# Performance work log

Hardware: AMD Instinct MI355X
Metric: run time of the kernel (lower is better)

The kernel has to match this reference:

```python
import jax, jax.numpy as jnp
import numpy as np
import itertools, math

METRIC = [1.0, 1.0, 1.0]  # Cl(3,0)
EPS = 1e-6
SQRT2 = math.sqrt(2.0)


def _build_algebra(metric):
    d = len(metric)
    # basis blades ordered by grade, then lexicographic combination (repo convention)
    blades = []
    for g in range(d + 1):
        for c in itertools.combinations(range(d), g):
            blades.append(sum(1 << i for i in c))
    idx = {m: i for i, m in enumerate(blades)}
    n = len(blades)
    C = np.zeros((n, n, n), dtype=np.float32)  # cayley[i, j, k]: e_i * e_k -> sign * e_j
    for ia, am in enumerate(blades):
        for ik, bm in enumerate(blades):
            a = am >> 1
            swaps = 0
            while a:
                swaps += bin(a & bm).count('1')
                a >>= 1
            sign = -1.0 if (swaps & 1) else 1.0
            for i in range(d):
                if am & bm & (1 << i):
                    sign *= metric[i]
            C[ia, idx[am ^ bm], ik] = sign
    grades = np.array([bin(m).count('1') for m in blades])
    subspaces = np.array([int((grades == g).sum()) for g in range(d + 1)])
    paths = np.zeros((d + 1, d + 1, d + 1), dtype=bool)
    for i in range(d + 1):
        for j in range(d + 1):
            for k in range(d + 1):
                paths[i, j, k] = np.any(C[np.ix_(grades == i, grades == j, grades == k)] != 0)
    return C, subspaces, paths, grades

CAYLEY_NP, SUBSPACES, PATHS, GRADE_OF_COMP = _build_algebra(METRIC)
REP_IDX = np.repeat(np.arange(len(SUBSPACES)), SUBSPACES)  # component -> grade, len 8
PI, PJ, PK = np.nonzero(PATHS)                              # 20 active grade triples
ONEHOT_GRADE = np.eye(len(SUBSPACES), dtype=np.float32)[GRADE_OF_COMP]  # [8,4]

B, N_IN, N_OUT = 1024, 256, 256
DIM_MV = CAYLEY_NP.shape[0]  # 8
N_PATHS = int(PATHS.sum())   # 20


def mv_linear(x, w, bias=None):
    # MVLinear: per-grade weight repeated over components; einsum 'bm...i,nmi->bn...i'
    wr = w[:, :, REP_IDX]                       # [out, in, 8]
    out = jnp.einsum('bmi,nmi->bni', x, wr)
    if bias is not None:
        out = out.at[:, :, 0].add(bias[:, :, 0])  # bias embedded in scalar (grade-0) slot
    return out


def normalize_mv(x, a):
    # per-grade norms (Euclidean metric => L2 norm of each grade block)
    oh = jnp.asarray(ONEHOT_GRADE)
    norms = jnp.sqrt(jnp.einsum('bni,ig->bng', x * x, oh))  # [b, n, 4]
    interp = jax.nn.sigmoid(a)[None] * (norms - 1.0) + 1.0  # learned interp toward unit norm
    return x / (interp[:, :, REP_IDX] + EPS)


def gp_kernel(gp_weight):
    # scatter 20 path weights into (m, n, 4, 4, 4), repeat per subspace, mask by cayley
    m, n, _ = gp_weight.shape
    g = len(SUBSPACES)
    w4 = jnp.zeros((m, n, g, g, g), gp_weight.dtype).at[:, :, PI, PJ, PK].set(gp_weight)
    wrep = w4[:, :, REP_IDX][:, :, :, REP_IDX][:, :, :, :, REP_IDX]  # [m, n, 8, 8, 8]
    return jnp.asarray(CAYLEY_NP)[None, None] * wrep


def setup_inputs() -> dict:
    key = jax.random.key(0)
    ks = jax.random.split(key, 5)
    std_gp = 1.0 / math.sqrt(N_IN * (len(METRIC) + 1))
    std_lin = 1.0 / math.sqrt(N_IN)
    return {
        'x': jax.random.normal(ks[0], (B, N_IN, DIM_MV), jnp.float32),
        'w_right': jax.random.normal(ks[1], (N_IN, N_IN, len(SUBSPACES)), jnp.float32) * std_lin,
        'w_left': jax.random.normal(ks[2], (N_OUT, N_IN, len(SUBSPACES)), jnp.float32) * std_lin,
        'b_left': jax.random.normal(ks[3], (1, N_OUT, 1), jnp.float32) * 0.02,
        'norm_a': jnp.zeros((N_IN, len(SUBSPACES)), jnp.float32),  # normalization_init = 0
        'gp_weight': jax.random.normal(ks[4], (N_OUT, N_IN, N_PATHS), jnp.float32) * std_gp,
    }


def reference(x, w_right, w_left, b_left, norm_a, gp_weight):
    x_right = normalize_mv(mv_linear(x, w_right), norm_a)
    kernel = gp_kernel(gp_weight)                 # [m, n, 8, 8, 8]
    outer = jnp.einsum('bni,bnk->bnik', x, x_right)  # [b, n, 8, 8]
    prod = jnp.einsum('bnik,mnijk->bmj', outer, kernel)
    left = mv_linear(x, w_left, b_left)
    return (left + prod) / SQRT2
```

## Files before the change

kernel.cpp:

```cpp
#include <hip/hip_runtime.h>
#include <math.h>

typedef unsigned short ushortT;
typedef __bf16 bf16x8 __attribute__((ext_vector_type(8)));
typedef float  f32x4  __attribute__((ext_vector_type(4)));

__constant__ int GRADEc[8] = {0,1,1,1,2,2,2,3};

__constant__ int CMAPc[8][7] = {
  {0, 8, 9,10,11, 0, 0},
  {1,12,13,14,15,16,17},
  {2,18,19,20,21,22,23},
  {3,24,25,26,27,28,29},
  {4,30,31,32,33,34,35},
  {5,36,37,38,39,40,41},
  {6,42,43,44,45,46,47},
  {7,48,49,50,51, 0, 0}};
__constant__ int WMAPc[8][7] = {
  {0, 4, 8,14,20, 0, 0},
  {1, 5, 9,10,15,16,21},
  {1, 5, 9,10,15,16,21},
  {1, 5, 9,10,15,16,21},
  {2, 6,11,12,17,18,22},
  {2, 6,11,12,17,18,22},
  {2, 6,11,12,17,18,22},
  {3, 7,13,19,23, 0, 0}};
__constant__ int SSTART2c[8][2] = {{0,3},{0,4},{0,4},{0,4},{0,4},{0,4},{0,4},{0,3}};
__constant__ int SCOUNT2c[8][2] = {{3,2},{4,3},{4,3},{4,3},{4,3},{4,3},{4,3},{3,2}};

__device__ __forceinline__ ushortT f2bf(float f) {
  unsigned int u = __float_as_uint(f);
  unsigned int r = (u + 0x7fffu + ((u >> 16) & 1u)) >> 16;
  return (ushortT)r;
}

#define GLOAD_LDS16(gsrc, ldst) \
  __builtin_amdgcn_global_load_lds((const __attribute__((address_space(1))) unsigned int*)(gsrc), \
                                   (__attribute__((address_space(3))) unsigned int*)(ldst), 16, 0, 0)

#define WAITVM(N) asm volatile("s_waitcnt vmcnt(" #N ")" ::: "memory")
#define SCHEDB()  __builtin_amdgcn_sched_barrier(0)
#define RAWBAR()  do { SCHEDB(); __builtin_amdgcn_s_barrier(); asm volatile("" ::: "memory"); SCHEDB(); } while (0)

__global__ void k_prep(const float* __restrict__ x, const float* __restrict__ w_right,
                       const float* __restrict__ w_left, const float* __restrict__ gp,
                       ushortT* __restrict__ XH, ushortT* __restrict__ XL,
                       ushortT* __restrict__ WH, ushortT* __restrict__ WL,
                       ushortT* __restrict__ WT2b) {
  const int bid = blockIdx.x;
  const int tid = threadIdx.x;
  if (bid < 256) {
    const int m = bid, n = tid;
    float4 wl = *(const float4*)(w_left + m * 1024 + n * 4);
    float g[20];
    const float4* gp4 = (const float4*)(gp + m * 5120 + n * 20);
    #pragma unroll
    for (int q = 0; q < 5; ++q) {
      float4 v = gp4[q];
      g[q * 4 + 0] = v.x; g[q * 4 + 1] = v.y; g[q * 4 + 2] = v.z; g[q * 4 + 3] = v.w;
    }
    const int base = m * 256 + n;
    WT2b[0 * 65536 + base] = f2bf(wl.x);
    WT2b[1 * 65536 + base] = f2bf(wl.y);
    WT2b[2 * 65536 + base] = f2bf(wl.z);
    WT2b[3 * 65536 + base] = f2bf(wl.w);
    #pragma unroll
    for (int p = 0; p < 20; ++p)
      WT2b[(4 + p) * 65536 + base] = f2bf(g[p]);
  } else if (bid < 1280) {
    int b = bid - 256;
    const float4* xp = (const float4*)(x + b * 2048 + tid * 8);
    float4 a = xp[0], c = xp[1];
    float v[8] = {a.x, a.y, a.z, a.w, c.x, c.y, c.z, c.w};
    #pragma unroll
    for (int i = 0; i < 8; ++i) {
      ushortT h = f2bf(v[i]);
      float hf = __uint_as_float(((unsigned int)h) << 16);
      XH[i * 262144 + b * 256 + tid] = h;
      XL[i * 262144 + b * 256 + tid] = f2bf(v[i] - hf);
    }
  } else {
    int n = bid - 1280;
    float4 w = *(const float4*)(w_right + n * 1024 + tid * 4);
    float v[4] = {w.x, w.y, w.z, w.w};
    #pragma unroll
    for (int g2 = 0; g2 < 4; ++g2) {
      ushortT h = f2bf(v[g2]);
      float hf = __uint_as_float(((unsigned int)h) << 16);
      WH[g2 * 65536 + n * 256 + tid] = h;
      WL[g2 * 65536 + n * 256 + tid] = f2bf(v[g2] - hf);
    }
  }
}

__global__ __launch_bounds__(512) void k_right_feat(const ushortT* __restrict__ XH,
                                                    const ushortT* __restrict__ XL,
                                                    const ushortT* __restrict__ WH,
                                                    const ushortT* __restrict__ WL,
                                                    const float* __restrict__ x,
                                                    const float* __restrict__ norm_a,
                                                    ushortT* __restrict__ FT2b) {
  const int lin = blockIdx.x;
  const int rr  = lin & 7;
  const int q   = lin >> 3;
  const int xb  = q & 7;
  const int yb  = (q >> 3) * 8 + rr;
  const int n0 = xb * 32;
  const int b0 = yb * 32;
  __shared__ __align__(16) ushortT lds[49152];
  const int t    = threadIdx.x;
  const int wave = t >> 6;
  const int lane = t & 63;
  const int i    = wave;
  const int g    = GRADEc[i];
  const int lrow = lane & 15, lkg = lane >> 4;
  const int srow = lane >> 2;
  const int sseg = lane & 3;

  const ushortT* Asrc_h = XH + i * 262144 + b0 * 256;
  const ushortT* Asrc_l = XL + i * 262144 + b0 * 256;
  const int bg = wave >> 1;
  const ushortT* Bsrc = ((wave & 1) ? WL : WH) + bg * 65536 + n0 * 256;

  f32x4 acc[2][2];
  #pragma unroll
  for (int r = 0; r < 2; ++r)
    #pragma unroll
    for (int c = 0; c < 2; ++c)
      acc[r][c] = (f32x4){0.f, 0.f, 0.f, 0.f};

  auto STAGE = [&](int k0, int buf) {
    ushortT* base = lds + buf * 24576;
    #pragma unroll
    for (int q2 = 0; q2 < 2; ++q2) {
      int row = q2 * 16 + srow;
      int slog = sseg ^ ((row >> 1) & 3);
      GLOAD_LDS16(Asrc_h + row * 256 + k0 + slog * 8, base + i * 1024 + q2 * 512);
      GLOAD_LDS16(Asrc_l + row * 256 + k0 + slog * 8, base + 8192 + i * 1024 + q2 * 512);
      GLOAD_LDS16(Bsrc   + row * 256 + k0 + slog * 8,
                  base + 16384 + (wave & 1) * 4096 + bg * 1024 + q2 * 512);
    }
  };

  auto COMPUTE = [&](int buf) {
    const ushortT* base = lds + buf * 24576;
    bf16x8 afh[2], afl[2], bfh[2], bfl[2];
    #pragma unroll
    for (int r = 0; r < 2; ++r) {
      int row = r * 16 + lrow;
      int po = row * 32 + (lkg ^ ((row >> 1) & 3)) * 8;
      afh[r] = *(const bf16x8*)(base + i * 1024 + po);
      afl[r] = *(const bf16x8*)(base + 8192 + i * 1024 + po);
    }
    #pragma unroll
    for (int c = 0; c < 2; ++c) {
      int row = c * 16 + lrow;
      int po = row * 32 + (lkg ^ ((row >> 1) & 3)) * 8;
      bfh[c] = *(const bf16x8*)(base + 16384 + g * 1024 + po);
      bfl[c] = *(const bf16x8*)(base + 20480 + g * 1024 + po);
    }
    #pragma unroll
    for (int r = 0; r < 2; ++r)
      #pragma unroll
      for (int c = 0; c < 2; ++c) {
        acc[r][c] = __builtin_amdgcn_mfma_f32_16x16x32_bf16(afh[r], bfh[c], acc[r][c], 0, 0, 0);
        acc[r][c] = __builtin_amdgcn_mfma_f32_16x16x32_bf16(afl[r], bfh[c], acc[r][c], 0, 0, 0);
        acc[r][c] = __builtin_amdgcn_mfma_f32_16x16x32_bf16(afh[r], bfl[c], acc[r][c], 0, 0, 0);
      }
  };

  STAGE(0, 0);
  int cur = 0;
  for (int tc = 0; tc < 8; ++tc) {
    if (tc < 7) { STAGE((tc + 1) * 32, cur ^ 1); SCHEDB(); WAITVM(6); }
    else        { WAITVM(0); }
    RAWBAR();
    COMPUTE(cur);
    if (tc < 7) RAWBAR();
    cur ^= 1;
  }

  float* yl = (float*)lds;
  #pragma unroll
  for (int r = 0; r < 2; ++r)
    #pragma unroll
    for (int c = 0; c < 2; ++c)
      #pragma unroll
      for (int e = 0; e < 4; ++e) {
        int row = r * 16 + lkg * 4 + e;
        int col = c * 16 + lrow;
        yl[i * 1056 + row * 33 + col] = acc[r][c][e];
      }
  __syncthreads();

  #pragma unroll
  for (int e2 = 0; e2 < 2; ++e2) {
    int el  = t + e2 * 512;
    int row = el >> 5, col = el & 31;
    int b = b0 + row, n = n0 + col;
    float y[8];
    #pragma unroll
    for (int q2 = 0; q2 < 8; ++q2) y[q2] = yl[q2 * 1056 + row * 33 + col];
    const float4* xp = (const float4*)(x + b * 2048 + n * 8);
    float4 x01 = xp[0], x23 = xp[1];
    float xv[8] = {x01.x, x01.y, x01.z, x01.w, x23.x, x23.y, x23.z, x23.w};
    float4 na = *(const float4*)(norm_a + n * 4);
    float nav[4] = {na.x, na.y, na.z, na.w};
    float nr[4];
    nr[0] = fabsf(y[0]);
    nr[1] = sqrtf(y[1]*y[1] + y[2]*y[2] + y[3]*y[3]);
    nr[2] = sqrtf(y[4]*y[4] + y[5]*y[5] + y[6]*y[6]);
    nr[3] = fabsf(y[7]);
    float inv[4];
    #pragma unroll
    for (int gg = 0; gg < 4; ++gg) {
      float s = 1.0f / (1.0f + expf(-nav[gg]));
      inv[gg] = 1.0f / (s * (nr[gg] - 1.0f) + 1.0f + 1e-6f);
    }
    float r[8];
    r[0] = y[0]*inv[0];
    r[1] = y[1]*inv[1]; r[2] = y[2]*inv[1]; r[3] = y[3]*inv[1];
    r[4] = y[4]*inv[2]; r[5] = y[5]*inv[2]; r[6] = y[6]*inv[2];
    r[7] = y[7]*inv[3];

    float F[52];
    F[8]  = xv[0]*r[0];
    F[9]  = xv[1]*r[1] + xv[2]*r[2] + xv[3]*r[3];
    F[10] = -(xv[4]*r[4] + xv[5]*r[5] + xv[6]*r[6]);
    F[11] = -xv[7]*r[7];
    F[12] = xv[0]*r[1];
    F[13] = xv[1]*r[0];
    F[14] = -(xv[2]*r[4] + xv[3]*r[5]);
    F[15] = xv[4]*r[2] + xv[5]*r[3];
    F[16] = -xv[6]*r[7];
    F[17] = -xv[7]*r[6];
    F[18] = xv[0]*r[2];
    F[19] = xv[2]*r[0];
    F[20] = xv[1]*r[4] - xv[3]*r[6];
    F[21] = -xv[4]*r[1] + xv[6]*r[3];
    F[22] = xv[5]*r[7];
    F[23] = xv[7]*r[5];
    F[24] = xv[0]*r[3];
    F[25] = xv[3]*r[0];
    F[26] = xv[1]*r[5] + xv[2]*r[6];
    F[27] = -(xv[5]*r[1] + xv[6]*r[2]);
    F[28] = -xv[4]*r[7];
    F[29] = -xv[7]*r[4];
    F[30] = xv[0]*r[4];
    F[31] = xv[1]*r[2] - xv[2]*r[1];
    F[32] = xv[3]*r[7];
    F[33] = xv[4]*r[0];
    F[34] = -xv[5]*r[6] + xv[6]*r[5];
    F[35] = xv[7]*r[3];
    F[36] = xv[0]*r[5];
    F[37] = xv[1]*r[3] - xv[3]*r[1];
    F[38] = -xv[2]*r[7];
    F[39] = xv[5]*r[0];
    F[40] = xv[4]*r[6] - xv[6]*r[4];
    F[41] = -xv[7]*r[2];
    F[42] = xv[0]*r[6];
    F[43] = xv[2]*r[3] - xv[3]*r[2];
    F[44] = xv[1]*r[7];
    F[45] = xv[6]*r[0];
    F[46] = -xv[4]*r[5] + xv[5]*r[4];
    F[47] = xv[7]*r[1];
    F[48] = xv[0]*r[7];
    F[49] = xv[1]*r[6] - xv[2]*r[5] + xv[3]*r[4];
    F[50] = xv[4]*r[3] - xv[5]*r[2] + xv[6]*r[1];
    F[51] = xv[7]*r[0];

    #pragma unroll
    for (int c = 8; c < 52; ++c)
      FT2b[c * 262144 + b * 256 + n] = f2bf(F[c]);
  }
}

__global__ __launch_bounds__(512) void k_gemm_mfma(const ushortT* __restrict__ XH,
                                                   const ushortT* __restrict__ FT2b,
                                                   const ushortT* __restrict__ WT2b,
                                                   float* __restrict__ outP) {
  const int lin = blockIdx.x;
  const int rr  = lin & 7;
  const int q   = lin >> 3;
  const int ix  = q & 15;
  const int z   = rr + 8 * (q >> 4);
  const int j   = z >> 1;
  const int ks  = z & 1;
  const int m0  = (ix & 1) * 128;
  const int b0  = (ix >> 1) * 128;
  __shared__ __align__(16) ushortT lds[32768];
  const int t    = threadIdx.x;
  const int wave = t >> 6;
  const int kkg  = wave >> 2;
  const int w4   = wave & 3;
  const int lane = t & 63;
  const int wb   = (w4 & 1) * 64;
  const int wm   = (w4 >> 1) * 64;
  const int lrow = lane & 15;
  const int lkg  = lane >> 4;
  const int srow = lane >> 3;
  const int sseg = lane & 7;

  f32x4 acc[4][4];
  #pragma unroll
  for (int r = 0; r < 4; ++r)
    #pragma unroll
    for (int c = 0; c < 4; ++c)
      acc[r][c] = (f32x4){0.f, 0.f, 0.f, 0.f};

  const int sstart = SSTART2c[j][ks];
  const int nt     = SCOUNT2c[j][ks] * 4;

  auto STAGE = [&](int tch, int buf) {
    int slot = sstart + (tch >> 2);
    int k0   = (tch & 3) << 6;
    const ushortT* Ap = ((slot == 0) ? (XH + j * 262144)
                                     : (FT2b + CMAPc[j][slot] * 262144)) + b0 * 256;
    const ushortT* Bp = WT2b + WMAPc[j][slot] * 65536 + m0 * 256;
    #pragma unroll
    for (int q2 = 0; q2 < 2; ++q2) {
      int idx = wave * 2 + q2;
      int row = idx * 8 + srow;
      int slog = sseg ^ (row & 7);
      GLOAD_LDS16(Ap + row * 256 + k0 + slog * 8, lds + buf * 8192 + idx * 512);
      GLOAD_LDS16(Bp + row * 256 + k0 + slog * 8, lds + 16384 + buf * 8192 + idx * 512);
    }
  };

  STAGE(0, 0);
  int cur = 0;
  for (int tc = 0; tc < nt; ++tc) {
    if (tc + 1 < nt) { STAGE(tc + 1, cur ^ 1); SCHEDB(); WAITVM(4); }
    else             { WAITVM(0); }
    RAWBAR();
    const ushortT* sA = lds + cur * 8192;
    const ushortT* sB = lds + 16384 + cur * 8192;
    bf16x8 af[4], bf[4];
    #pragma unroll
    for (int r = 0; r < 4; ++r) {
      int row = wb + r * 16 + lrow;
      af[r] = *(const bf16x8*)(sA + row * 64 + (((kkg * 4 + lkg) ^ (row & 7)) * 8));
    }
    #pragma unroll
    for (int c = 0; c < 4; ++c) {
      int row = wm + c * 16 + lrow;
      bf[c] = *(const bf16x8*)(sB + row * 64 + (((kkg * 4 + lkg) ^ (row & 7)) * 8));
    }
    #pragma unroll
    for (int r = 0; r < 4; ++r)
      #pragma unroll
      for (int c = 0; c < 4; ++c)
        acc[r][c] = __builtin_amdgcn_mfma_f32_16x16x32_bf16(af[r], bf[c], acc[r][c], 0, 0, 0);
    if (tc + 1 < nt) RAWBAR();
    cur ^= 1;
  }

  __syncthreads();
  float* fl = (float*)lds;
  if (kkg == 1) {
    #pragma unroll
    for (int r = 0; r < 4; ++r)
      #pragma unroll
      for (int c = 0; c < 4; ++c)
        #pragma unroll
        for (int e = 0; e < 4; ++e) {
          int row = r * 16 + lkg * 4 + e;
          int col = c * 16 + lrow;
          fl[w4 * 4096 + row * 64 + col] = acc[r][c][e];
        }
  }
  __syncthreads();
  if (kkg == 0) {
    float* oj = outP + (ks * 8 + j) * 262144;
    #pragma unroll
    for (int r = 0; r < 4; ++r) {
      #pragma unroll
      for (int c = 0; c < 4; ++c) {
        #pragma unroll
        for (int e = 0; e < 4; ++e) {
          int row = r * 16 + lkg * 4 + e;
          int col = c * 16 + lrow;
          float v = acc[r][c][e] + fl[w4 * 4096 + row * 64 + col];
          oj[(b0 + wb + row) * 256 + m0 + wm + col] = v;
        }
      }
    }
  }
}

__global__ void k_merge(const float* __restrict__ outP, const float* __restrict__ bleft,
                        float* __restrict__ out) {
  const int t4 = (blockIdx.x * 256 + threadIdx.x) * 4;
  const int m  = t4 & 255;
  const float sc = 0.7071067811865475f;
  float o[4][8];
  #pragma unroll
  for (int jj = 0; jj < 8; ++jj) {
    float4 s = make_float4(0.f, 0.f, 0.f, 0.f);
    #pragma unroll
    for (int p = 0; p < 2; ++p) {
      float4 v = *(const float4*)(outP + (p * 8 + jj) * 262144 + t4);
      s.x += v.x; s.y += v.y; s.z += v.z; s.w += v.w;
    }
    o[0][jj] = s.x; o[1][jj] = s.y; o[2][jj] = s.z; o[3][jj] = s.w;
  }
  #pragma unroll
  for (int q = 0; q < 4; ++q) {
    float ov[8];
    #pragma unroll
    for (int jj = 0; jj < 8; ++jj) ov[jj] = o[q][jj];
    ov[0] += bleft[m + q];
    float4 v0 = make_float4(ov[0]*sc, ov[1]*sc, ov[2]*sc, ov[3]*sc);
    float4 v1 = make_float4(ov[4]*sc, ov[5]*sc, ov[6]*sc, ov[7]*sc);
    *(float4*)(out + (t4 + q) * 8)     = v0;
    *(float4*)(out + (t4 + q) * 8 + 4) = v1;
  }
}

extern "C" void kernel_launch(void* const* d_in, const int* in_sizes, int n_in,
                              void* d_out, int out_size, void* d_ws, size_t ws_size,
                              hipStream_t stream) {
  const float* x       = (const float*)d_in[0];
  const float* w_right = (const float*)d_in[1];
  const float* w_left  = (const float*)d_in[2];
  const float* b_left  = (const float*)d_in[3];
  const float* norm_a  = (const float*)d_in[4];
  const float* gp      = (const float*)d_in[5];
  float* out = (float*)d_out;
  float* W   = (float*)d_ws;

  float*   outP = W;
  ushortT* XH   = (ushortT*)(W + 4194304);
  ushortT* XL   = (ushortT*)(W + 5242880);
  ushortT* WH   = (ushortT*)(W + 6291456);
  ushortT* WL   = (ushortT*)(W + 6422528);
  ushortT* FT2b = (ushortT*)(W + 6553600);
  ushortT* WT2b = (ushortT*)(W + 13369344);

  k_prep<<<1536, 256, 0, stream>>>(x, w_right, w_left, gp, XH, XL, WH, WL, WT2b);
  k_right_feat<<<256, 512, 0, stream>>>(XH, XL, WH, WL, x, norm_a, FT2b);
  k_gemm_mfma<<<256, 512, 0, stream>>>(XH, FT2b, WT2b, outP);
  k_merge<<<256, 256, 0, stream>>>(outP, b_left, out);
}
```

Baseline: 109.9 us.

## Fuse four kernels into one cooperative kernel with grid syncs

Merges the prep, right-feature GEMM, main GEMM and merge kernels into a single cooperative launch of 256 blocks of 512 threads, separated by grid-wide barriers. This removes three kernel launch gaps and the tail/ramp between stages. In exchange, the prep and merge stages run with fewer, larger blocks doing strided loops, all stages share one LDS allocation sized for the largest, and grid.sync adds barrier cost.

```diff
diff --git a/kernel.cpp b/kernel.cpp
--- a/kernel.cpp
+++ b/kernel.cpp
@@ -1,5 +1,8 @@
 #include <hip/hip_runtime.h>
+#include <hip/hip_cooperative_groups.h>
 #include <math.h>
+
+namespace cg = cooperative_groups;
 
 typedef unsigned short ushortT;
 typedef __bf16 bf16x8 __attribute__((ext_vector_type(8)));
@@ -42,378 +45,386 @@
 #define SCHEDB()  __builtin_amdgcn_sched_barrier(0)
 #define RAWBAR()  do { SCHEDB(); __builtin_amdgcn_s_barrier(); asm volatile("" ::: "memory"); SCHEDB(); } while (0)
 
-__global__ void k_prep(const float* __restrict__ x, const float* __restrict__ w_right,
-                       const float* __restrict__ w_left, const float* __restrict__ gp,
-                       ushortT* __restrict__ XH, ushortT* __restrict__ XL,
-                       ushortT* __restrict__ WH, ushortT* __restrict__ WL,
-                       ushortT* __restrict__ WT2b) {
+__global__ __launch_bounds__(512, 2) void k_fused(
+    const float* __restrict__ x, const float* __restrict__ w_right,
+    const float* __restrict__ w_left, const float* __restrict__ bleft,
+    const float* __restrict__ norm_a, const float* __restrict__ gp,
+    float* __restrict__ out,
+    ushortT* __restrict__ XH, ushortT* __restrict__ XL,
+    ushortT* __restrict__ WH, ushortT* __restrict__ WL,
+    ushortT* __restrict__ FT2b, ushortT* __restrict__ WT2b,
+    float* __restrict__ outP) {
+  cg::grid_group grid = cg::this_grid();
+  __shared__ __align__(16) ushortT lds[49152];
   const int bid = blockIdx.x;
   const int tid = threadIdx.x;
-  if (bid < 256) {
-    const int m = bid, n = tid;
-    float4 wl = *(const float4*)(w_left + m * 1024 + n * 4);
-    float g[20];
-    const float4* gp4 = (const float4*)(gp + m * 5120 + n * 20);
+
+  {
     #pragma unroll
-    for (int q = 0; q < 5; ++q) {
-      float4 v = gp4[q];
-      g[q * 4 + 0] = v.x; g[q * 4 + 1] = v.y; g[q * 4 + 2] = v.z; g[q * 4 + 3] = v.w;
-    }
-    const int base = m * 256 + n;
-    WT2b[0 * 65536 + base] = f2bf(wl.x);
-    WT2b[1 * 65536 + base] = f2bf(wl.y);
-    WT2b[2 * 65536 + base] = f2bf(wl.z);
-    WT2b[3 * 65536 + base] = f2bf(wl.w);
-    #pragma unroll
-    for (int p = 0; p < 20; ++p)
-      WT2b[(4 + p) * 65536 + base] = f2bf(g[p]);
-  } else if (bid < 1280) {
-    int b = bid - 256;
-    const float4* xp = (const float4*)(x + b * 2048 + tid * 8);
-    float4 a = xp[0], c = xp[1];
-    float v[8] = {a.x, a.y, a.z, a.w, c.x, c.y, c.z, c.w};
-    #pragma unroll
-    for (int i = 0; i < 8; ++i) {
-      ushortT h = f2bf(v[i]);
-      float hf = __uint_as_float(((unsigned int)h) << 16);
-      XH[i * 262144 + b * 256 + tid] = h;
-      XL[i * 262144 + b * 256 + tid] = f2bf(v[i] - hf);
-    }
-  } else {
-    int n = bid - 1280;
-    float4 w = *(const float4*)(w_right + n * 1024 + tid * 4);
-    float v[4] = {w.x, w.y, w.z, w.w};
-    #pragma unroll
-    for (int g2 = 0; g2 < 4; ++g2) {
-      ushortT h = f2bf(v[g2]);
-      float hf = __uint_as_float(((unsigned int)h) << 16);
-      WH[g2 * 65536 + n * 256 + tid] = h;
-      WL[g2 * 65536 + n * 256 + tid] = f2bf(v[g2] - hf);
+    for (int k = 0; k < 3; ++k) {
+      int u  = k * 131072 + bid * 512 + tid;
+      int vb = u >> 8, vt = u & 255;
+      if (vb < 256) {
+        const int m = vb, n = vt;
+        float4 wl = *(const float4*)(w_left + m * 1024 + n * 4);
+        float g[20];
+        const float4* gp4 = (const float4*)(gp + m * 5120 + n * 20);
+        #pragma unroll
+        for (int q = 0; q < 5; ++q) {
+          float4 v = gp4[q];
+          g[q * 4 + 0] = v.x; g[q * 4 + 1] = v.y; g[q * 4 + 2] = v.z; g[q * 4 + 3] = v.w;
+        }
+        const int base = m * 256 + n;
+        WT2b[0 * 65536 + base] = f2bf(wl.x);
+        WT2b[1 * 65536 + base] = f2bf(wl.y);
+        WT2b[2 * 65536 + base] = f2bf(wl.z);
+        WT2b[3 * 65536 + base] = f2bf(wl.w);
+        #pragma unroll
+        for (int p = 0; p < 20; ++p)
+          WT2b[(4 + p) * 65536 + base] = f2bf(g[p]);
+      } else if (vb < 1280) {
+        int b = vb - 256;
+        const float4* xp = (const float4*)(x + b * 2048 + vt * 8);
+        float4 a = xp[0], c = xp[1];
+        float v[8] = {a.x, a.y, a.z, a.w, c.x, c.y, c.z, c.w};
+        #pragma unroll
+        for (int i = 0; i < 8; ++i) {
+          ushortT h = f2bf(v[i]);
+          float hf = __uint_as_float(((unsigned int)h) << 16);
+          XH[i * 262144 + b * 256 + vt] = h;
+          XL[i * 262144 + b * 256 + vt] = f2bf(v[i] - hf);
+        }
+      } else {
+        int n = vb - 1280;
+        float4 w = *(const float4*)(w_right + n * 1024 + vt * 4);
+        float v[4] = {w.x, w.y, w.z, w.w};
+        #pragma unroll
+        for (int g2 = 0; g2 < 4; ++g2) {
+          ushortT h = f2bf(v[g2]);
+          float hf = __uint_as_float(((unsigned int)h) << 16);
+          WH[g2 * 65536 + n * 256 + vt] = h;
+          WL[g2 * 65536 + n * 256 + vt] = f2bf(v[g2] - hf);
+        }
+      }
     }
   }
-}
-
-__global__ __launch_bounds__(512) void k_right_feat(const ushortT* __restrict__ XH,
-                                                    const ushortT* __restrict__ XL,
-                                                    const ushortT* __restrict__ WH,
-                                                    const ushortT* __restrict__ WL,
-                                                    const float* __restrict__ x,
-                                                    const float* __restrict__ norm_a,
-                                                    ushortT* __restrict__ FT2b) {
-  const int lin = blockIdx.x;
-  const int rr  = lin & 7;
-  const int q   = lin >> 3;
-  const int xb  = q & 7;
-  const int yb  = (q >> 3) * 8 + rr;
-  const int n0 = xb * 32;
-  const int b0 = yb * 32;
-  __shared__ __align__(16) ushortT lds[49152];
-  const int t    = threadIdx.x;
-  const int wave = t >> 6;
-  const int lane = t & 63;
-  const int i    = wave;
-  const int g    = GRADEc[i];
-  const int lrow = lane & 15, lkg = lane >> 4;
-  const int srow = lane >> 2;
-  const int sseg = lane & 3;
-
-  const ushortT* Asrc_h = XH + i * 262144 + b0 * 256;
-  const ushortT* Asrc_l = XL + i * 262144 + b0 * 256;
-  const int bg = wave >> 1;
-  const ushortT* Bsrc = ((wave & 1) ? WL : WH) + bg * 65536 + n0 * 256;
-
-  f32x4 acc[2][2];
-  #pragma unroll
-  for (int r = 0; r < 2; ++r)
-    #pragma unroll
-    for (int c = 0; c < 2; ++c)
-      acc[r][c] = (f32x4){0.f, 0.f, 0.f, 0.f};
-
-  auto STAGE = [&](int k0, int buf) {
-    ushortT* base = lds + buf * 24576;
-    #pragma unroll
-    for (int q2 = 0; q2 < 2; ++q2) {
-      int row = q2 * 16 + srow;
-      int slog = sseg ^ ((row >> 1) & 3);
-      GLOAD_LDS16(Asrc_h + row * 256 + k0 + slog * 8, base + i * 1024 + q2 * 512);
-      GLOAD_LDS16(Asrc_l + row * 256 + k0 + slog * 8, base + 8192 + i * 1024 + q2 * 512);
-      GLOAD_LDS16(Bsrc   + row * 256 + k0 + slog * 8,
-                  base + 16384 + (wave & 1) * 4096 + bg * 1024 + q2 * 512);
-    }
-  };
-
-  auto COMPUTE = [&](int buf) {
-    const ushortT* base = lds + buf * 24576;
-    bf16x8 afh[2], afl[2], bfh[2], bfl[2];
-    #pragma unroll
-    for (int r = 0; r < 2; ++r) {
-      int row = r * 16 + lrow;
-      int po = row * 32 + (lkg ^ ((row >> 1) & 3)) * 8;
-      afh[r] = *(const bf16x8*)(base + i * 1024 + po);
-      afl[r] = *(const bf16x8*)(base + 8192 + i * 1024 + po);
-    }
-    #pragma unroll
-    for (int c = 0; c < 2; ++c) {
-      int row = c * 16 + lrow;
-      int po = row * 32 + (lkg ^ ((row >> 1) & 3)) * 8;
-      bfh[c] = *(const bf16x8*)(base + 16384 + g * 1024 + po);
-      bfl[c] = *(const bf16x8*)(base + 20480 + g * 1024 + po);
-    }
+  grid.sync();
+
+  {
+    const int lin = bid;
+    const int rr  = lin & 7;
+    const int q   = lin >> 3;
+    const int xb  = q & 7;
+    const int yb  = (q >> 3) * 8 + rr;
+    const int n0 = xb * 32;
+    const int b0 = yb * 32;
+    const int t    = tid;
+    const int wave = t >> 6;
+    const int lane = t & 63;
+    const int i    = wave;
+    const int g    = GRADEc[i];
+    const int lrow = lane & 15, lkg = lane >> 4;
+    const int srow = lane >> 2;
+    const int sseg = lane & 3;
+
+    const ushortT* Asrc_h = XH + i * 262144 + b0 * 256;
+    const ushortT* Asrc_l = XL + i * 262144 + b0 * 256;
+    const int bg = wave >> 1;
+    const ushortT* Bsrc = ((wave & 1) ? WL : WH) + bg * 65536 + n0 * 256;
+
+    f32x4 acc[2][2];
     #pragma unroll
     for (int r = 0; r < 2; ++r)
       #pragma unroll
+      for (int c = 0; c < 2; ++c)
+        acc[r][c] = (f32x4){0.f, 0.f, 0.f, 0.f};
+
+    auto STAGE = [&](int k0, int buf) {
+      ushortT* base = lds + buf * 24576;
+      #pragma unroll
+      for (int q2 = 0; q2 < 2; ++q2) {
+        int row = q2 * 16 + srow;
+        int slog = sseg ^ ((row >> 1) & 3);
+        GLOAD_LDS16(Asrc_h + row * 256 + k0 + slog * 8, base + i * 1024 + q2 * 512);
+        GLOAD_LDS16(Asrc_l + row * 256 + k0 + slog * 8, base + 8192 + i * 1024 + q2 * 512);
+        GLOAD_LDS16(Bsrc   + row * 256 + k0 + slog * 8,
+                    base + 16384 + (wave & 1) * 4096 + bg * 1024 + q2 * 512);
+      }
+    };
+
+    auto COMPUTE = [&](int buf) {
+      const ushortT* base = lds + buf * 24576;
+      bf16x8 afh[2], afl[2], bfh[2], bfl[2];
+      #pragma unroll
+      for (int r = 0; r < 2; ++r) {
+        int row = r * 16 + lrow;
+        int po = row * 32 + (lkg ^ ((row >> 1) & 3)) * 8;
+        afh[r] = *(const bf16x8*)(base + i * 1024 + po);
+        afl[r] = *(const bf16x8*)(base + 8192 + i * 1024 + po);
+      }
+      #pragma unroll
       for (int c = 0; c < 2; ++c) {
-        acc[r][c] = __builtin_amdgcn_mfma_f32_16x16x32_bf16(afh[r], bfh[c], acc[r][c], 0, 0, 0);
-        acc[r][c] = __builtin_amdgcn_mfma_f32_16x16x32_bf16(afl[r], bfh[c], acc[r][c], 0, 0, 0);
-        acc[r][c] = __builtin_amdgcn_mfma_f32_16x16x32_bf16(afh[r], bfl[c], acc[r][c], 0, 0, 0);
-      }
-  };
-
-  STAGE(0, 0);
-  int cur = 0;
-  for (int tc = 0; tc < 8; ++tc) {
-    if (tc < 7) { STAGE((tc + 1) * 32, cur ^ 1); SCHEDB(); WAITVM(6); }
-    else        { WAITVM(0); }
-    RAWBAR();
-    COMPUTE(cur);
-    if (tc < 7) RAWBAR();
-    cur ^= 1;
-  }
-
-  float* yl = (float*)lds;
-  #pragma unroll
-  for (int r = 0; r < 2; ++r)
+        int row = c * 16 + lrow;
+        int po = row * 32 + (lkg ^ ((row >> 1) & 3)) * 8;
+        bfh[c] = *(const bf16x8*)(base + 16384 + g * 1024 + po);
+        bfl[c] = *(const bf16x8*)(base + 20480 + g * 1024 + po);
+      }
+      #pragma unroll
+      for (int r = 0; r < 2; ++r)
+        #pragma unroll
+        for (int c = 0; c < 2; ++c) {
+          acc[r][c] = __builtin_amdgcn_mfma_f32_16x16x32_bf16(afh[r], bfh[c], acc[r][c], 0, 0, 0);
+          acc[r][c] = __builtin_amdgcn_mfma_f32_16x16x32_bf16(afl[r], bfh[c], acc[r][c], 0, 0, 0);
+          acc[r][c] = __builtin_amdgcn_mfma_f32_16x16x32_bf16(afh[r], bfl[c], acc[r][c], 0, 0, 0);
+        }
+    };
+
+    STAGE(0, 0);
+    int cur = 0;
+    for (int tc = 0; tc < 8; ++tc) {
+      if (tc < 7) { STAGE((tc + 1) * 32, cur ^ 1); SCHEDB(); WAITVM(6); }
+      else        { WAITVM(0); }
+      RAWBAR();
+      COMPUTE(cur);
+      if (tc < 7) RAWBAR();
+      cur ^= 1;
+    }
+
+    float* yl = (float*)lds;
     #pragma unroll
-    for (int c = 0; c < 2; ++c)
-      #pragma unroll
-      for (int e = 0; e < 4; ++e) {
-        int row = r * 16 + lkg * 4 + e;
-        int col = c * 16 + lrow;
-        yl[i * 1056 + row * 33 + col] = acc[r][c][e];
-      }
-  __syncthreads();
-
-  #pragma unroll
-  for (int e2 = 0; e2 < 2; ++e2) {
-    int el  = t + e2 * 512;
-    int row = el >> 5, col = el & 31;
-    int b = b0 + row, n = n0 + col;
-    float y[8];
-    #pragma unroll
-    for (int q2 = 0; q2 < 8; ++q2) y[q2] = yl[q2 * 1056 + row * 33 + col];
-    const float4* xp = (const float4*)(x + b * 2048 + n * 8);
-    float4 x01 = xp[0], x23 = xp[1];
-    float xv[8] = {x01.x, x01.y, x01.z, x01.w, x23.x, x23.y, x23.z, x23.w};
-    float4 na = *(const float4*)(norm_a + n * 4);
-    float nav[4] = {na.x, na.y, na.z, na.w};
-    float nr[4];
-    nr[0] = fabsf(y[0]);
-    nr[1] = sqrtf(y[1]*y[1] + y[2]*y[2] + y[3]*y[3]);
-    nr[2] = sqrtf(y[4]*y[4] + y[5]*y[5] + y[6]*y[6]);
-    nr[3] = fabsf(y[7]);
-    float inv[4];
-    #pragma unroll
-    for (int gg = 0; gg < 4; ++gg) {
-      float s = 1.0f / (1.0f + expf(-nav[gg]));
-      inv[gg] = 1.0f / (s * (nr[gg] - 1.0f) + 1.0f + 1e-6f);
-    }
-    float r[8];
-    r[0] = y[0]*inv[0];
-    r[1] = y[1]*inv[1]; r[2] = y[2]*inv[1]; r[3] = y[3]*inv[1];
-    r[4] = y[4]*inv[2]; r[5] = y[5]*inv[2]; r[6] = y[6]*inv[2];
-    r[7] = y[7]*inv[3];
-
-    float F[52];
-    F[8]  = xv[0]*r[0];
-    F[9]  = xv[1]*r[1] + xv[2]*r[2] + xv[3]*r[3];
-    F[10] = -(xv[4]*r[4] + xv[5]*r[5] + xv[6]*r[6]);
-    F[11] = -xv[7]*r[7];
-    F[12] = xv[0]*r[1];
-    F[13] = xv[1]*r[0];
-    F[14] = -(xv[2]*r[4] + xv[3]*r[5]);
-    F[15] = xv[4]*r[2] + xv[5]*r[3];
-    F[16] = -xv[6]*r[7];
-    F[17] = -xv[7]*r[6];
-    F[18] = xv[0]*r[2];
-    F[19] = xv[2]*r[0];
-    F[20] = xv[1]*r[4] - xv[3]*r[6];
-    F[21] = -xv[4]*r[1] + xv[6]*r[3];
-    F[22] = xv[5]*r[7];
-    F[23] = xv[7]*r[5];
-    F[24] = xv[0]*r[3];
-    F[25] = xv[3]*r[0];
-    F[26] = xv[1]*r[5] + xv[2]*r[6];
-    F[27] = -(xv[5]*r[1] + xv[6]*r[2]);
-    F[28] = -xv[4]*r[7];
-    F[29] = -xv[7]*r[4];
-    F[30] = xv[0]*r[4];
-    F[31] = xv[1]*r[2] - xv[2]*r[1];
-    F[32] = xv[3]*r[7];
-    F[33] = xv[4]*r[0];
-    F[34] = -xv[5]*r[6] + xv[6]*r[5];
-    F[35] = xv[7]*r[3];
-    F[36] = xv[0]*r[5];
-    F[37] = xv[1]*r[3] - xv[3]*r[1];
-    F[38] = -xv[2]*r[7];
-    F[39] = xv[5]*r[0];
-    F[40] = xv[4]*r[6] - xv[6]*r[4];
-    F[41] = -xv[7]*r[2];
-    F[42] = xv[0]*r[6];
-    F[43] = xv[2]*r[3] - xv[3]*r[2];
-    F[44] = xv[1]*r[7];
-    F[45] = xv[6]*r[0];
-    F[46] = -xv[4]*r[5] + xv[5]*r[4];
-    F[47] = xv[7]*r[1];
-    F[48] = xv[0]*r[7];
-    F[49] = xv[1]*r[6] - xv[2]*r[5] + xv[3]*r[4];
-    F[50] = xv[4]*r[3] - xv[5]*r[2] + xv[6]*r[1];
-    F[51] = xv[7]*r[0];
-
-    #pragma unroll
-    for (int c = 8; c < 52; ++c)
-      FT2b[c * 262144 + b * 256 + n] = f2bf(F[c]);
-  }
-}
-
-__global__ __launch_bounds__(512) void k_gemm_mfma(const ushortT* __restrict__ XH,
-                                                   const ushortT* __restrict__ FT2b,
-                                                   const ushortT* __restrict__ WT2b,
-                                                   float* __restrict__ outP) {
-  const int lin = blockIdx.x;
-  const int rr  = lin & 7;
-  const int q   = lin >> 3;
-  const int ix  = q & 15;
-  const int z   = rr + 8 * (q >> 4);
-  const int j   = z >> 1;
-  const int ks  = z & 1;
-  const int m0  = (ix & 1) * 128;
-  const int b0  = (ix >> 1) * 128;
-  __shared__ __align__(16) ushortT lds[32768];
-  const int t    = threadIdx.x;
-  const int wave = t >> 6;
-  const int kkg  = wave >> 2;
-  const int w4   = wave & 3;
-  const int lane = t & 63;
-  const int wb   = (w4 & 1) * 64;
-  const int wm   = (w4 >> 1) * 64;
-  const int lrow = lane & 15;
-  const int lkg  = lane >> 4;
-  const int srow = lane >> 3;
-  const int sseg = lane & 7;
-
-  f32x4 acc[4][4];
-  #pragma unroll
-  for (int r = 0; r < 4; ++r)
-    #pragma unroll
-    for (int c = 0; c < 4; ++c)
-      acc[r][c] = (f32x4){0.f, 0.f, 0.f, 0.f};
-
-  const int sstart = SSTART2c[j][ks];
-  const int nt     = SCOUNT2c[j][ks] * 4;
-
-  auto STAGE = [&](int tch, int buf) {
-    int slot = sstart + (tch >> 2);
-    int k0   = (tch & 3) << 6;
-    const ushortT* Ap = ((slot == 0) ? (XH + j * 262144)
-                                     : (FT2b + CMAPc[j][slot] * 262144)) + b0 * 256;
-    const ushortT* Bp = WT2b + WMAPc[j][slot] * 65536 + m0 * 256;
-    #pragma unroll
-    for (int q2 = 0; q2 < 2; ++q2) {
-      int idx = wave * 2 + q2;
-      int row = idx * 8 + srow;
-      int slog = sseg ^ (row & 7);
-      GLOAD_LDS16(Ap + row * 256 + k0 + slog * 8, lds + buf * 8192 + idx * 512);
-      GLOAD_LDS16(Bp + row * 256 + k0 + slog * 8, lds + 16384 + buf * 8192 + idx * 512);
-    }
-  };
-
-  STAGE(0, 0);
-  int cur = 0;
-  for (int tc = 0; tc < nt; ++tc) {
-    if (tc + 1 < nt) { STAGE(tc + 1, cur ^ 1); SCHEDB(); WAITVM(4); }
-    else             { WAITVM(0); }
-    RAWBAR();
-    const ushortT* sA = lds + cur * 8192;
-    const ushortT* sB = lds + 16384 + cur * 8192;
-    bf16x8 af[4], bf[4];
-    #pragma unroll
-    for (int r = 0; r < 4; ++r) {
-      int row = wb + r * 16 + lrow;
-      af[r] = *(const bf16x8*)(sA + row * 64 + (((kkg * 4 + lkg) ^ (row & 7)) * 8));
-    }
-    #pragma unroll
-    for (int c = 0; c < 4; ++c) {
-      int row = wm + c * 16 + lrow;
-      bf[c] = *(const bf16x8*)(sB + row * 64 + (((kkg * 4 + lkg) ^ (row & 7)) * 8));
-    }
-    #pragma unroll
-    for (int r = 0; r < 4; ++r)
-      #pragma unroll
-      for (int c = 0; c < 4; ++c)
-        acc[r][c] = __builtin_amdgcn_mfma_f32_16x16x32_bf16(af[r], bf[c], acc[r][c], 0, 0, 0);
-    if (tc + 1 < nt) RAWBAR();
-    cur ^= 1;
-  }
-
-  __syncthreads();
-  float* fl = (float*)lds;
-  if (kkg == 1) {
-    #pragma unroll
-    for (int r = 0; r < 4; ++r)
-      #pragma unroll
-      for (int c = 0; c < 4; ++c)
+    for (int r = 0; r < 2; ++r)
+      #pragma unroll
+      for (int c = 0; c < 2; ++c)
         #pragma unroll
         for (int e = 0; e < 4; ++e) {
           int row = r * 16 + lkg * 4 + e;
           int col = c * 16 + lrow;
-          fl[w4 * 4096 + row * 64 + col] = acc[r][c][e];
-        }
+          yl[i * 1056 + row * 33 + col] = acc[r][c][e];
+        }
+    __syncthreads();
+
+    #pragma unroll
+    for (int e2 = 0; e2 < 2; ++e2) {
+      int el  = t + e2 * 512;
+      int row = el >> 5, col = el & 31;
+      int b = b0 + row, n = n0 + col;
+      float y[8];
+      #pragma unroll
+      for (int q2 = 0; q2 < 8; ++q2) y[q2] = yl[q2 * 1056 + row * 33 + col];
+      const float4* xp = (const float4*)(x + b * 2048 + n * 8);
+      float4 x01 = xp[0], x23 = xp[1];
+      float xv[8] = {x01.x, x01.y, x01.z, x01.w, x23.x, x23.y, x23.z, x23.w};
+      float4 na = *(const float4*)(norm_a + n * 4);
+      float nav[4] = {na.x, na.y, na.z, na.w};
+      float nr[4];
+      nr[0] = fabsf(y[0]);
+      nr[1] = sqrtf(y[1]*y[1] + y[2]*y[2] + y[3]*y[3]);
+      nr[2] = sqrtf(y[4]*y[4] + y[5]*y[5] + y[6]*y[6]);
+      nr[3] = fabsf(y[7]);
+      float inv[4];
+      #pragma unroll
+      for (int gg = 0; gg < 4; ++gg) {
+        float s = 1.0f / (1.0f + expf(-nav[gg]));
+        inv[gg] = 1.0f / (s * (nr[gg] - 1.0f) + 1.0f + 1e-6f);
+      }
+      float r[8];
+      r[0] = y[0]*inv[0];
+      r[1] = y[1]*inv[1]; r[2] = y[2]*inv[1]; r[3] = y[3]*inv[1];
+      r[4] = y[4]*inv[2]; r[5] = y[5]*inv[2]; r[6] = y[6]*inv[2];
+      r[7] = y[7]*inv[3];
+
+      float F[52];
+      F[8]  = xv[0]*r[0];
+      F[9]  = xv[1]*r[1] + xv[2]*r[2] + xv[3]*r[3];
+      F[10] = -(xv[4]*r[4] + xv[5]*r[5] + xv[6]*r[6]);
+      F[11] = -xv[7]*r[7];
+      F[12] = xv[0]*r[1];
+      F[13] = xv[1]*r[0];
+      F[14] = -(xv[2]*r[4] + xv[3]*r[5]);
+      F[15] = xv[4]*r[2] + xv[5]*r[3];
+      F[16] = -xv[6]*r[7];
+      F[17] = -xv[7]*r[6];
+      F[18] = xv[0]*r[2];
+      F[19] = xv[2]*r[0];
+      F[20] = xv[1]*r[4] - xv[3]*r[6];
+      F[21] = -xv[4]*r[1] + xv[6]*r[3];
+      F[22] = xv[5]*r[7];
+      F[23] = xv[7]*r[5];
+      F[24] = xv[0]*r[3];
+      F[25] = xv[3]*r[0];
+      F[26] = xv[1]*r[5] + xv[2]*r[6];
+      F[27] = -(xv[5]*r[1] + xv[6]*r[2]);
+      F[28] = -xv[4]*r[7];
+      F[29] = -xv[7]*r[4];
+      F[30] = xv[0]*r[4];
+      F[31] = xv[1]*r[2] - xv[2]*r[1];
+      F[32] = xv[3]*r[7];
+      F[33] = xv[4]*r[0];
+      F[34] = -xv[5]*r[6] + xv[6]*r[5];
+      F[35] = xv[7]*r[3];
+      F[36] = xv[0]*r[5];
+      F[37] = xv[1]*r[3] - xv[3]*r[1];
+      F[38] = -xv[2]*r[7];
+      F[39] = xv[5]*r[0];
+      F[40] = xv[4]*r[6] - xv[6]*r[4];
+      F[41] = -xv[7]*r[2];
+      F[42] = xv[0]*r[6];
+      F[43] = xv[2]*r[3] - xv[3]*r[2];
+      F[44] = xv[1]*r[7];
+      F[45] = xv[6]*r[0];
+      F[46] = -xv[4]*r[5] + xv[5]*r[4];
+      F[47] = xv[7]*r[1];
+      F[48] = xv[0]*r[7];
+      F[49] = xv[1]*r[6] - xv[2]*r[5] + xv[3]*r[4];
+      F[50] = xv[4]*r[3] - xv[5]*r[2] + xv[6]*r[1];
+      F[51] = xv[7]*r[0];
+
+      #pragma unroll
+      for (int c = 8; c < 52; ++c)
+        FT2b[c * 262144 + b * 256 + n] = f2bf(F[c]);
+    }
   }
-  __syncthreads();
-  if (kkg == 0) {
-    float* oj = outP + (ks * 8 + j) * 262144;
+  grid.sync();
+
+  {
+    const int lin = bid;
+    const int rr  = lin & 7;
+    const int q   = lin >> 3;
+    const int ix  = q & 15;
+    const int z   = rr + 8 * (q >> 4);
+    const int j   = z >> 1;
+    const int ks  = z & 1;
+    const int m0  = (ix & 1) * 128;
+    const int b0  = (ix >> 1) * 128;
+    const int t    = tid;
+    const int wave = t >> 6;
+    const int kkg  = wave >> 2;
+    const int w4   = wave & 3;
+    const int lane = t & 63;
+    const int wb   = (w4 & 1) * 64;
+    const int wm   = (w4 >> 1) * 64;
+    const int lrow = lane & 15;
+    const int lkg  = lane >> 4;
+    const int srow = lane >> 3;
+    const int sseg = lane & 7;
+
+    f32x4 acc[4][4];
     #pragma unroll
-    for (int r = 0; r < 4; ++r) {
+    for (int r = 0; r < 4; ++r)
+      #pragma unroll
+      for (int c = 0; c < 4; ++c)
+        acc[r][c] = (f32x4){0.f, 0.f, 0.f, 0.f};
+
+    const int sstart = SSTART2c[j][ks];
+    const int nt     = SCOUNT2c[j][ks] * 4;
+
+    auto STAGE = [&](int tch, int buf) {
+      int slot = sstart + (tch >> 2);
+      int k0   = (tch & 3) << 6;
+      const ushortT* Ap = ((slot == 0) ? (XH + j * 262144)
+                                       : (FT2b + CMAPc[j][slot] * 262144)) + b0 * 256;
+      const ushortT* Bp = WT2b + WMAPc[j][slot] * 65536 + m0 * 256;
+      #pragma unroll
+      for (int q2 = 0; q2 < 2; ++q2) {
+        int idx = wave * 2 + q2;
+        int row = idx * 8 + srow;
+        int slog = sseg ^ (row & 7);
+        GLOAD_LDS16(Ap + row * 256 + k0 + slog * 8, lds + buf * 8192 + idx * 512);
+        GLOAD_LDS16(Bp + row * 256 + k0 + slog * 8, lds + 16384 + buf * 8192 + idx * 512);
+      }
+    };
+
+    STAGE(0, 0);
+    int cur = 0;
+    for (int tc = 0; tc < nt; ++tc) {
+      if (tc + 1 < nt) { STAGE(tc + 1, cur ^ 1); SCHEDB(); WAITVM(4); }
+      else             { WAITVM(0); }
+      RAWBAR();
+      const ushortT* sA = lds + cur * 8192;
+      const ushortT* sB = lds + 16384 + cur * 8192;
+      bf16x8 af[4], bf[4];
+      #pragma unroll
+      for (int r = 0; r < 4; ++r) {
+        int row = wb + r * 16 + lrow;
+        af[r] = *(const bf16x8*)(sA + row * 64 + (((kkg * 4 + lkg) ^ (row & 7)) * 8));
+      }
       #pragma unroll
       for (int c = 0; c < 4; ++c) {
-        #pragma unroll
-        for (int e = 0; e < 4; ++e) {
-          int row = r * 16 + lkg * 4 + e;
-          int col = c * 16 + lrow;
-          float v = acc[r][c][e] + fl[w4 * 4096 + row * 64 + col];
-          oj[(b0 + wb + row) * 256 + m0 + wm + col] = v;
+        int row = wm + c * 16 + lrow;
+        bf[c] = *(const bf16x8*)(sB + row * 64 + (((kkg * 4 + lkg) ^ (row & 7)) * 8));
+      }
+      #pragma unroll
+      for (int r = 0; r < 4; ++r)
+        #pragma unroll
+        for (int c = 0; c < 4; ++c)
+          acc[r][c] = __builtin_amdgcn_mfma_f32_16x16x32_bf16(af[r], bf[c], acc[r][c], 0, 0, 0);
+      if (tc + 1 < nt) RAWBAR();
+      cur ^= 1;
+    }
+
+    __syncthreads();
+    float* fl = (float*)lds;
+    if (kkg == 1) {
+      #pragma unroll
+      for (int r = 0; r < 4; ++r)
+        #pragma unroll
+        for (int c = 0; c < 4; ++c)
+          #pragma unroll
+          for (int e = 0; e < 4; ++e) {
+            int row = r * 16 + lkg * 4 + e;
+            int col = c * 16 + lrow;
+            fl[w4 * 4096 + row * 64 + col] = acc[r][c][e];
+          }
+    }
+    __syncthreads();
+    if (kkg == 0) {
+      float* oj = outP + (ks * 8 + j) * 262144;
+      #pragma unroll
+      for (int r = 0; r < 4; ++r) {
+        #pragma unroll
+        for (int c = 0; c < 4; ++c) {
+          #pragma unroll
+          for (int e = 0; e < 4; ++e) {
+            int row = r * 16 + lkg * 4 + e;
+            int col = c * 16 + lrow;
+            float v = acc[r][c][e] + fl[w4 * 4096 + row * 64 + col];
+            oj[(b0 + wb + row) * 256 + m0 + wm + col] = v;
+          }
         }
       }
     }
   }
-}
-
-__global__ void k_merge(const float* __restrict__ outP, const float* __restrict__ bleft,
-                        float* __restrict__ out) {
-  const int t4 = (blockIdx.x * 256 + threadIdx.x) * 4;
-  const int m  = t4 & 255;
-  const float sc = 0.7071067811865475f;
-  float o[4][8];
-  #pragma unroll
-  for (int jj = 0; jj < 8; ++jj) {
-    float4 s = make_float4(0.f, 0.f, 0.f, 0.f);
-    #pragma unroll
-    for (int p = 0; p < 2; ++p) {
-      float4 v = *(const float4*)(outP + (p * 8 + jj) * 262144 + t4);
-      s.x += v.x; s.y += v.y; s.z += v.z; s.w += v.w;
-    }
-    o[0][jj] = s.x; o[1][jj] = s.y; o[2][jj] = s.z; o[3][jj] = s.w;
-  }
-  #pragma unroll
-  for (int q = 0; q < 4; ++q) {
-    float ov[8];
-    #pragma unroll
-    for (int jj = 0; jj < 8; ++jj) ov[jj] = o[q][jj];
-    ov[0] += bleft[m + q];
-    float4 v0 = make_float4(ov[0]*sc, ov[1]*sc, ov[2]*sc, ov[3]*sc);
-    float4 v1 = make_float4(ov[4]*sc, ov[5]*sc, ov[6]*sc, ov[7]*sc);
-    *(float4*)(out + (t4 + q) * 8)     = v0;
-    *(float4*)(out + (t4 + q) * 8 + 4) = v1;
+  grid.sync();
+
+  {
+    const int gtid = bid * 512 + tid;
+    if (gtid < 65536) {
+      const int t4 = gtid * 4;
+      const int m  = t4 & 255;
+      const float sc = 0.7071067811865475f;
+      float o[4][8];
+      #pragma unroll
+      for (int jj = 0; jj < 8; ++jj) {
+        float4 s = make_float4(0.f, 0.f, 0.f, 0.f);
+        #pragma unroll
+        for (int p = 0; p < 2; ++p) {
+          float4 v = *(const float4*)(outP + (p * 8 + jj) * 262144 + t4);
+          s.x += v.x; s.y += v.y; s.z += v.z; s.w += v.w;
+        }
+        o[0][jj] = s.x; o[1][jj] = s.y; o[2][jj] = s.z; o[3][jj] = s.w;
+      }
+      #pragma unroll
+      for (int q = 0; q < 4; ++q) {
+        float ov[8];
+        #pragma unroll
+        for (int jj = 0; jj < 8; ++jj) ov[jj] = o[q][jj];
+        ov[0] += bleft[m + q];
+        float4 v0 = make_float4(ov[0]*sc, ov[1]*sc, ov[2]*sc, ov[3]*sc);
+        float4 v1 = make_float4(ov[4]*sc, ov[5]*sc, ov[6]*sc, ov[7]*sc);
+        *(float4*)(out + (t4 + q) * 8)     = v0;
+        *(float4*)(out + (t4 + q) * 8 + 4) = v1;
+      }
+    }
   }
 }
 
@@ -437,8 +448,9 @@
   ushortT* FT2b = (ushortT*)(W + 6553600);
   ushortT* WT2b = (ushortT*)(W + 13369344);
 
-  k_prep<<<1536, 256, 0, stream>>>(x, w_right, w_left, gp, XH, XL, WH, WL, WT2b);
-  k_right_feat<<<256, 512, 0, stream>>>(XH, XL, WH, WL, x, norm_a, FT2b);
-  k_gemm_mfma<<<256, 512, 0, stream>>>(XH, FT2b, WT2b, outP);
-  k_merge<<<256, 256, 0, stream>>>(outP, b_left, out);
+  void* args[] = { (void*)&x, (void*)&w_right, (void*)&w_left, (void*)&b_left,
+                   (void*)&norm_a, (void*)&gp, (void*)&out,
+                   (void*)&XH, (void*)&XL, (void*)&WH, (void*)&WL,
+                   (void*)&FT2b, (void*)&WT2b, (void*)&outP };
+  hipLaunchCooperativeKernel((const void*)k_fused, dim3(256), dim3(512), args, 0, stream);
 }
```

Result: slower. 228.0 us (+107.5%).
